# Optimization experiments

Hardware: AMD Instinct MI355X
Metric: run time of the kernel (lower is better)

The kernel has to match this reference:

```python
import jax, jax.numpy as jnp
import numpy as np

N_EMBD = 1024
NUM_HEADS = 16
HEAD_SIZE = 64


def setup_inputs() -> dict:
    key = jax.random.key(0)
    ks = jax.random.split(key, 6)
    B, T, C, hs = 2, 2048, N_EMBD, HEAD_SIZE
    s = 0.02
    return {
        "x": jax.random.normal(ks[0], (B, T, C), dtype=jnp.float32),
        "Wk": jax.random.normal(ks[1], (hs, C), dtype=jnp.float32) * s,  # torch Linear weight [out,in]
        "Wv": jax.random.normal(ks[2], (hs, C), dtype=jnp.float32) * s,
        "Wq": jax.random.normal(ks[3], (C, C), dtype=jnp.float32) * s,
        "Wp": jax.random.normal(ks[4], (C, C), dtype=jnp.float32) * s,
        "bp": jax.random.normal(ks[5], (C,), dtype=jnp.float32) * s,
    }


def reference(x, Wk, Wv, Wq, Wp, bp):
    B, T, C = x.shape
    H, hs = NUM_HEADS, HEAD_SIZE
    k = x @ Wk.T                      # [B,T,hs]
    v = x @ Wv.T                      # [B,T,hs]
    q = x @ Wq.T                      # [B,T,C]
    # Faithful to torch: raw view of [B,T,C] -> [B,H,T,hs] (row-major reshape, not transpose)
    q = q.reshape(B, H, T, hs)
    k = k.reshape(B, 1, T, hs)
    v = v.reshape(B, 1, T, hs)
    att = jnp.einsum("bhqd,bhkd->bhqk", q, jnp.broadcast_to(k, (B, 1, T, hs))) * (hs ** -0.5)
    mask = jnp.tril(jnp.ones((T, T), dtype=bool))[None, None]  # [1,1,T,T]
    att = jnp.where(mask, att, -jnp.inf)
    att = jax.nn.softmax(att, axis=-1)
    y = jnp.einsum("bhqk,bhkd->bhqd", att, jnp.broadcast_to(v, (B, 1, T, hs)))  # [B,H,T,hs]
    y = jnp.transpose(y, (0, 2, 1, 3)).reshape(B, T, C)
    return y @ Wp.T + bp
```

## Files before the change

### kernel.cpp

```cpp
#include <hip/hip_runtime.h>
#include <cstddef>
#include <cstdint>

#define B_N 2
#define T_N 2048
#define C_N 1024
#define H_N 16
#define HS_N 64
#define M_N (B_N * T_N)

typedef __attribute__((ext_vector_type(8))) short bf16x8;
typedef __attribute__((ext_vector_type(4))) float f32x4;

#define QSCALE 0.18033688011112042f

__device__ __forceinline__ ushort f2bf(float f) {
    union { float f; uint32_t u; } v; v.f = f;
    uint32_t r = v.u + 0x7fffu + ((v.u >> 16) & 1u);
    return (ushort)(r >> 16);
}

__global__ void cvt_all_kernel(const float* __restrict__ x,
                               const float* __restrict__ Wq,
                               const float* __restrict__ Wp,
                               const float* __restrict__ Wk,
                               const float* __restrict__ Wv,
                               ushort* __restrict__ xb,
                               ushort* __restrict__ Wqb,
                               ushort* __restrict__ Wpb,
                               ushort* __restrict__ Wkvb) {
    const int S0 = M_N * C_N / 4;
    const int S1 = S0 + C_N * C_N / 4;
    const int S2 = S1 + C_N * C_N / 4;
    const int S3 = S2 + HS_N * C_N / 4;
    const int S4 = S3 + HS_N * C_N / 4;
    const int stride = gridDim.x * blockDim.x;
    for (int i = blockIdx.x * blockDim.x + threadIdx.x; i < S4; i += stride) {
        const float* src; ushort* dst; int j; float sc = 1.f;
        if (i < S0)      { src = x;  dst = xb;   j = i; }
        else if (i < S1) { src = Wq; dst = Wqb;  j = i - S0; sc = QSCALE; }
        else if (i < S2) { src = Wp; dst = Wpb;  j = i - S1; }
        else if (i < S3) { src = Wk; dst = Wkvb; j = i - S2; }
        else             { src = Wv; dst = Wkvb + HS_N * C_N; j = i - S3; }
        const float4 f = ((const float4*)src)[j];
        ushort4 o;
        o.x = f2bf(f.x * sc); o.y = f2bf(f.y * sc);
        o.z = f2bf(f.z * sc); o.w = f2bf(f.w * sc);
        ((ushort4*)dst)[j] = o;
    }
}

template <bool BF16_OUT>
__global__ __launch_bounds__(256) void gemm_bf16_mfma(
    const ushort* __restrict__ A,
    const ushort* __restrict__ W,
    const float* __restrict__ bias,
    void* __restrict__ Cout,
    ushort* __restrict__ Cout2,
    int Nsplit, int N2, int K)
{
    __shared__ ushort As[128][72];
    __shared__ ushort Bs[64][72];
    const int m0 = blockIdx.x * 128;
    const int n0 = blockIdx.y * 64;
    const int tid = threadIdx.x;
    const int wid = tid >> 6;
    const int lane = tid & 63;
    const int ln = lane & 15;
    const int quad = lane >> 4;
    const int wm = wid >> 1, wn = wid & 1;

    f32x4 acc[4][2];
    #pragma unroll
    for (int i = 0; i < 4; ++i)
        #pragma unroll
        for (int j = 0; j < 2; ++j)
            acc[i][j] = (f32x4){0.f, 0.f, 0.f, 0.f};

    const int r0 = tid >> 2;
    const int c0 = tid & 3;
    const ushort* agA = A + (size_t)(m0 + r0) * K + c0 * 8;
    const ushort* agB = A + (size_t)(m0 + r0 + 64) * K + c0 * 8;
    const ushort* wg  = W + (size_t)(n0 + r0) * K + c0 * 8;

    int4 pa0, pa1, pa2, pa3, pb0, pb1;
    {
        pa0 = *(const int4*)(agA);      pa1 = *(const int4*)(agA + 32);
        pa2 = *(const int4*)(agB);      pa3 = *(const int4*)(agB + 32);
        pb0 = *(const int4*)(wg);       pb1 = *(const int4*)(wg + 32);
    }

    for (int k0 = 0; k0 < K; k0 += 64) {
        __syncthreads();
        *(int4*)&As[r0][c0 * 8]           = pa0;
        *(int4*)&As[r0][c0 * 8 + 32]      = pa1;
        *(int4*)&As[r0 + 64][c0 * 8]      = pa2;
        *(int4*)&As[r0 + 64][c0 * 8 + 32] = pa3;
        *(int4*)&Bs[r0][c0 * 8]           = pb0;
        *(int4*)&Bs[r0][c0 * 8 + 32]      = pb1;
        __syncthreads();
        const int kn = k0 + 64;
        if (kn < K) {
            pa0 = *(const int4*)(agA + kn);      pa1 = *(const int4*)(agA + kn + 32);
            pa2 = *(const int4*)(agB + kn);      pa3 = *(const int4*)(agB + kn + 32);
            pb0 = *(const int4*)(wg + kn);       pb1 = *(const int4*)(wg + kn + 32);
        }
        #pragma unroll
        for (int hh = 0; hh < 2; ++hh) {
            bf16x8 af[4], bf[2];
            #pragma unroll
            for (int i = 0; i < 4; ++i)
                af[i] = *(const bf16x8*)&As[wm * 64 + i * 16 + ln][hh * 32 + quad * 8];
            #pragma unroll
            for (int j = 0; j < 2; ++j)
                bf[j] = *(const bf16x8*)&Bs[wn * 32 + j * 16 + ln][hh * 32 + quad * 8];
            #pragma unroll
            for (int i = 0; i < 4; ++i)
                #pragma unroll
                for (int j = 0; j < 2; ++j)
                    acc[i][j] = __builtin_amdgcn_mfma_f32_16x16x32_bf16(
                        af[i], bf[j], acc[i][j], 0, 0, 0);
        }
    }

    const bool side2 = (n0 >= Nsplit);
    #pragma unroll
    for (int i = 0; i < 4; ++i) {
        #pragma unroll
        for (int j = 0; j < 2; ++j) {
            const int col = n0 + wn * 32 + j * 16 + ln;
            const float bv = (!side2 && bias) ? bias[col] : 0.f;
            #pragma unroll
            for (int reg = 0; reg < 4; ++reg) {
                const int row = m0 + wm * 64 + i * 16 + quad * 4 + reg;
                const float v = acc[i][j][reg] + bv;
                if (side2)
                    Cout2[(size_t)row * N2 + (col - Nsplit)] = f2bf(v);
                else if (BF16_OUT)
                    ((ushort*)Cout)[(size_t)row * Nsplit + col] = f2bf(v);
                else
                    ((float*)Cout)[(size_t)row * Nsplit + col] = v;
            }
        }
    }
}

__global__ __launch_bounds__(256) void attn_mfma_kernel(
    const ushort* __restrict__ qb,
    const ushort* __restrict__ kvb,
    ushort* __restrict__ yb)
{
    __shared__ ushort Ks[64][72];
    __shared__ ushort Vt[64][72];
    __shared__ ushort Ps[4][16][72];

    const int bh = blockIdx.x;
    const int b = bh >> 4, h = bh & 15;
    const int p = blockIdx.y;
    const int lastB = 31 - p;
    const int qA0 = p * 64;
    const int qB0 = lastB * 64;
    const int tid = threadIdx.x;
    const int wid = tid >> 6;
    const int lane = tid & 63;
    const int ln = lane & 15;
    const int quad = lane >> 4;

    const ushort* qstrip = qb + (size_t)b * T_N * C_N + (size_t)h * T_N * HS_N;
    const size_t qrA = (size_t)(qA0 + wid * 16 + ln) * HS_N;
    const size_t qrB = (size_t)(qB0 + wid * 16 + ln) * HS_N;
    const bf16x8 qfA0 = *(const bf16x8*)(qstrip + qrA + quad * 8);
    const bf16x8 qfA1 = *(const bf16x8*)(qstrip + qrA + 32 + quad * 8);
    const bf16x8 qfB0 = *(const bf16x8*)(qstrip + qrB + quad * 8);
    const bf16x8 qfB1 = *(const bf16x8*)(qstrip + qrB + 32 + quad * 8);

    f32x4 oA[4], oB[4];
    float lA[4] = {0.f, 0.f, 0.f, 0.f};
    float lB[4] = {0.f, 0.f, 0.f, 0.f};
    #pragma unroll
    for (int nt = 0; nt < 4; ++nt) {
        oA[nt] = (f32x4){0.f, 0.f, 0.f, 0.f};
        oB[nt] = (f32x4){0.f, 0.f, 0.f, 0.f};
    }

    const ushort* kvbase = kvb + (size_t)b * T_N * 128;
    const int rs = tid >> 3;
    const int cs = tid & 7;

    int4 kc0, kc1, vc0, vc1;
    {
        const ushort* g0 = kvbase + (size_t)rs * 128 + cs * 8;
        kc0 = *(const int4*)g0;
        kc1 = *(const int4*)(g0 + 32 * 128);
        vc0 = *(const int4*)(g0 + 64);
        vc1 = *(const int4*)(g0 + 32 * 128 + 64);
    }

    auto compute_tile = [&](const bf16x8& qf0, const bf16x8& qf1,
                            f32x4* o, float* l, int qt0, int k0, bool diag) {
        f32x4 s[4];
        #pragma unroll
        for (int nt = 0; nt < 4; ++nt) {
            s[nt] = (f32x4){0.f, 0.f, 0.f, 0.f};
            const bf16x8 kf0 = *(const bf16x8*)&Ks[nt * 16 + ln][quad * 8];
            const bf16x8 kf1 = *(const bf16x8*)&Ks[nt * 16 + ln][32 + quad * 8];
            s[nt] = __builtin_amdgcn_mfma_f32_16x16x32_bf16(qf0, kf0, s[nt], 0, 0, 0);
            s[nt] = __builtin_amdgcn_mfma_f32_16x16x32_bf16(qf1, kf1, s[nt], 0, 0, 0);
        }
        #pragma unroll
        for (int reg = 0; reg < 4; ++reg) {
            const int qg = qt0 + wid * 16 + quad * 4 + reg;
            const int prow = quad * 4 + reg;
            const int psw = (prow >> 1) & 7;
            #pragma unroll
            for (int nt = 0; nt < 4; ++nt) {
                float sv = s[nt][reg];
                if (diag && (k0 + nt * 16 + ln > qg)) sv = -1e30f;
                const float pe = __builtin_amdgcn_exp2f(sv);
                l[reg] += pe;
                Ps[wid][prow][((2 * nt + (ln >> 3)) ^ psw) * 8 + (ln & 7)] = f2bf(pe);
            }
        }
        #pragma unroll
        for (int ks2 = 0; ks2 < 2; ++ks2) {
            const int rsw = (ln >> 1) & 7;
            const bf16x8 pf = *(const bf16x8*)&Ps[wid][ln][((ks2 * 4 + quad) ^ rsw) * 8];
            #pragma unroll
            for (int nt = 0; nt < 4; ++nt) {
                const int vsw = (2 * nt + (ln >> 3)) & 7;
                const bf16x8 vf = *(const bf16x8*)&Vt[nt * 16 + ln][((quad + 4 * ks2) ^ vsw) * 8];
                o[nt] = __builtin_amdgcn_mfma_f32_16x16x32_bf16(pf, vf, o[nt], 0, 0, 0);
            }
        }
    };

    for (int kt = 0; kt <= lastB; ++kt) {
        const int k0 = kt * 64;
        __syncthreads();
        *(int4*)&Ks[rs][cs * 8] = kc0;
        *(int4*)&Ks[rs + 32][cs * 8] = kc1;
        {
            const ushort* p0 = (const ushort*)&vc0;
            const ushort* p1 = (const ushort*)&vc1;
            const int pc0 = ((rs >> 3) ^ cs) * 8 + (rs & 7);
            const int pc1 = (((rs + 32) >> 3) ^ cs) * 8 + (rs & 7);
            #pragma unroll
            for (int i = 0; i < 8; ++i) {
                Vt[cs * 8 + i][pc0] = p0[i];
                Vt[cs * 8 + i][pc1] = p1[i];
            }
        }
        __syncthreads();
        if (kt < lastB) {
            const ushort* g0 = kvbase + (size_t)(k0 + 64 + rs) * 128 + cs * 8;
            kc0 = *(const int4*)g0;
            kc1 = *(const int4*)(g0 + 32 * 128);
            vc0 = *(const int4*)(g0 + 64);
            vc1 = *(const int4*)(g0 + 32 * 128 + 64);
        }
        compute_tile(qfB0, qfB1, oB, lB, qB0, k0, kt == lastB);
        if (kt <= p)
            compute_tile(qfA0, qfA1, oA, lA, qA0, k0, kt == p);
    }

    #pragma unroll
    for (int reg = 0; reg < 4; ++reg) {
        float la = lA[reg], lb = lB[reg];
        la += __shfl_xor(la, 1); lb += __shfl_xor(lb, 1);
        la += __shfl_xor(la, 2); lb += __shfl_xor(lb, 2);
        la += __shfl_xor(la, 4); lb += __shfl_xor(lb, 4);
        la += __shfl_xor(la, 8); lb += __shfl_xor(lb, 8);
        const float invA = 1.0f / la;
        const float invB = 1.0f / lb;
        const int qgA = qA0 + wid * 16 + quad * 4 + reg;
        const int qgB = qB0 + wid * 16 + quad * 4 + reg;
        ushort* yrA = yb + (size_t)b * T_N * C_N + (size_t)qgA * C_N + h * HS_N;
        ushort* yrB = yb + (size_t)b * T_N * C_N + (size_t)qgB * C_N + h * HS_N;
        #pragma unroll
        for (int nt = 0; nt < 4; ++nt) {
            yrA[nt * 16 + ln] = f2bf(oA[nt][reg] * invA);
            yrB[nt * 16 + ln] = f2bf(oB[nt][reg] * invB);
        }
    }
}

extern "C" void kernel_launch(void* const* d_in, const int* in_sizes, int n_in,
                              void* d_out, int out_size, void* d_ws, size_t ws_size,
                              hipStream_t stream) {
    const float* x  = (const float*)d_in[0];
    const float* Wk = (const float*)d_in[1];
    const float* Wv = (const float*)d_in[2];
    const float* Wq = (const float*)d_in[3];
    const float* Wp = (const float*)d_in[4];
    const float* bp = (const float*)d_in[5];
    float* out = (float*)d_out;

    ushort* xb   = (ushort*)d_ws;
    ushort* qb   = xb   + (size_t)M_N * C_N;
    ushort* yb   = qb   + (size_t)M_N * C_N;
    ushort* kvb  = yb   + (size_t)M_N * C_N;
    ushort* Wqb  = kvb  + (size_t)M_N * 128;
    ushort* Wkvb = Wqb  + (size_t)C_N * C_N;
    ushort* Wpb  = Wkvb + (size_t)128 * C_N;

    cvt_all_kernel<<<1024, 256, 0, stream>>>(x, Wq, Wp, Wk, Wv,
                                             xb, Wqb, Wpb, Wkvb);

    gemm_bf16_mfma<true><<<dim3(M_N / 128, (C_N + 128) / 64), 256, 0, stream>>>(
        xb, Wqb, nullptr, qb, kvb, C_N, 128, C_N);

    attn_mfma_kernel<<<dim3(B_N * H_N, 16), 256, 0, stream>>>(qb, kvb, yb);

    gemm_bf16_mfma<false><<<dim3(M_N / 128, C_N / 64), 256, 0, stream>>>(
        yb, Wpb, bp, out, nullptr, C_N, 0, C_N);
}
```

Baseline: 168.4 us.

## Use direct global-to-LDS loads in GEMM and widen attention query tiles

The GEMM now stages A and W tiles through global_load_lds with an XOR-swizzled unpadded LDS layout, replacing the register prefetch. That removes the register round trip but loses the overlap of next-tile loads with compute. The attention kernel now gives each block two 128-row query strips (two 16-row sub-tiles per wave) and hoists the K/V fragments into registers once per key tile. It also computes S transposed, so P can be written with packed stores. This halves the grid and raises register pressure (launch_bounds 256,1) in exchange for more K/V reuse per LDS load.

```diff
diff --git a/kernel.cpp b/kernel.cpp
--- a/kernel.cpp
+++ b/kernel.cpp
@@ -19,6 +19,11 @@
     uint32_t r = v.u + 0x7fffu + ((v.u >> 16) & 1u);
     return (ushort)(r >> 16);
 }
+
+#define GLL16(g, l)                                                         \
+    __builtin_amdgcn_global_load_lds(                                       \
+        (const __attribute__((address_space(1))) unsigned int*)(g),         \
+        (__attribute__((address_space(3))) unsigned int*)(l), 16, 0, 0)
 
 __global__ void cvt_all_kernel(const float* __restrict__ x,
                                const float* __restrict__ Wq,
@@ -59,8 +64,8 @@
     ushort* __restrict__ Cout2,
     int Nsplit, int N2, int K)
 {
-    __shared__ ushort As[128][72];
-    __shared__ ushort Bs[64][72];
+    __shared__ ushort As[128 * 64];
+    __shared__ ushort Bs[64 * 64];
     const int m0 = blockIdx.x * 128;
     const int n0 = blockIdx.y * 64;
     const int tid = threadIdx.x;
@@ -77,43 +82,39 @@
         for (int j = 0; j < 2; ++j)
             acc[i][j] = (f32x4){0.f, 0.f, 0.f, 0.f};
 
-    const int r0 = tid >> 2;
-    const int c0 = tid & 3;
-    const ushort* agA = A + (size_t)(m0 + r0) * K + c0 * 8;
-    const ushort* agB = A + (size_t)(m0 + r0 + 64) * K + c0 * 8;
-    const ushort* wg  = W + (size_t)(n0 + r0) * K + c0 * 8;
-
-    int4 pa0, pa1, pa2, pa3, pb0, pb1;
-    {
-        pa0 = *(const int4*)(agA);      pa1 = *(const int4*)(agA + 32);
-        pa2 = *(const int4*)(agB);      pa3 = *(const int4*)(agB + 32);
-        pb0 = *(const int4*)(wg);       pb1 = *(const int4*)(wg + 32);
-    }
+    const int srow = lane >> 3;
+    const int schk = (lane & 7) ^ srow;
 
     for (int k0 = 0; k0 < K; k0 += 64) {
         __syncthreads();
-        *(int4*)&As[r0][c0 * 8]           = pa0;
-        *(int4*)&As[r0][c0 * 8 + 32]      = pa1;
-        *(int4*)&As[r0 + 64][c0 * 8]      = pa2;
-        *(int4*)&As[r0 + 64][c0 * 8 + 32] = pa3;
-        *(int4*)&Bs[r0][c0 * 8]           = pb0;
-        *(int4*)&Bs[r0][c0 * 8 + 32]      = pb1;
+        #pragma unroll
+        for (int t = 0; t < 4; ++t) {
+            const int seg = wid * 4 + t;
+            const int row = seg * 8 + srow;
+            GLL16(A + (size_t)(m0 + row) * K + k0 + schk * 8, As + seg * 512);
+        }
+        #pragma unroll
+        for (int t = 0; t < 2; ++t) {
+            const int seg = wid * 2 + t;
+            const int row = seg * 8 + srow;
+            GLL16(W + (size_t)(n0 + row) * K + k0 + schk * 8, Bs + seg * 512);
+        }
         __syncthreads();
-        const int kn = k0 + 64;
-        if (kn < K) {
-            pa0 = *(const int4*)(agA + kn);      pa1 = *(const int4*)(agA + kn + 32);
-            pa2 = *(const int4*)(agB + kn);      pa3 = *(const int4*)(agB + kn + 32);
-            pb0 = *(const int4*)(wg + kn);       pb1 = *(const int4*)(wg + kn + 32);
-        }
+
         #pragma unroll
         for (int hh = 0; hh < 2; ++hh) {
             bf16x8 af[4], bf[2];
-            #pragma unroll
-            for (int i = 0; i < 4; ++i)
-                af[i] = *(const bf16x8*)&As[wm * 64 + i * 16 + ln][hh * 32 + quad * 8];
-            #pragma unroll
-            for (int j = 0; j < 2; ++j)
-                bf[j] = *(const bf16x8*)&Bs[wn * 32 + j * 16 + ln][hh * 32 + quad * 8];
+            const int sw = ln & 7;
+            #pragma unroll
+            for (int i = 0; i < 4; ++i) {
+                const int row = wm * 64 + i * 16 + ln;
+                af[i] = *(const bf16x8*)&As[row * 64 + (((hh * 4 + quad) ^ sw) * 8)];
+            }
+            #pragma unroll
+            for (int j = 0; j < 2; ++j) {
+                const int row = wn * 32 + j * 16 + ln;
+                bf[j] = *(const bf16x8*)&Bs[row * 64 + (((hh * 4 + quad) ^ sw) * 8)];
+            }
             #pragma unroll
             for (int i = 0; i < 4; ++i)
                 #pragma unroll
@@ -145,21 +146,20 @@
     }
 }
 
-__global__ __launch_bounds__(256) void attn_mfma_kernel(
+__global__ __launch_bounds__(256, 1) void attn_mfma_kernel(
     const ushort* __restrict__ qb,
     const ushort* __restrict__ kvb,
     ushort* __restrict__ yb)
 {
     __shared__ ushort Ks[64][72];
     __shared__ ushort Vt[64][72];
-    __shared__ ushort Ps[4][16][72];
+    __shared__ ushort Ps[8][16][72];
 
     const int bh = blockIdx.x;
     const int b = bh >> 4, h = bh & 15;
     const int p = blockIdx.y;
-    const int lastB = 31 - p;
-    const int qA0 = p * 64;
-    const int qB0 = lastB * 64;
+    const int qB0 = (15 - p) * 128;
+    const int qA0 = p * 128;
     const int tid = threadIdx.x;
     const int wid = tid >> 6;
     const int lane = tid & 63;
@@ -167,21 +167,26 @@
     const int quad = lane >> 4;
 
     const ushort* qstrip = qb + (size_t)b * T_N * C_N + (size_t)h * T_N * HS_N;
-    const size_t qrA = (size_t)(qA0 + wid * 16 + ln) * HS_N;
-    const size_t qrB = (size_t)(qB0 + wid * 16 + ln) * HS_N;
-    const bf16x8 qfA0 = *(const bf16x8*)(qstrip + qrA + quad * 8);
-    const bf16x8 qfA1 = *(const bf16x8*)(qstrip + qrA + 32 + quad * 8);
-    const bf16x8 qfB0 = *(const bf16x8*)(qstrip + qrB + quad * 8);
-    const bf16x8 qfB1 = *(const bf16x8*)(qstrip + qrB + 32 + quad * 8);
-
-    f32x4 oA[4], oB[4];
-    float lA[4] = {0.f, 0.f, 0.f, 0.f};
-    float lB[4] = {0.f, 0.f, 0.f, 0.f};
-    #pragma unroll
-    for (int nt = 0; nt < 4; ++nt) {
-        oA[nt] = (f32x4){0.f, 0.f, 0.f, 0.f};
-        oB[nt] = (f32x4){0.f, 0.f, 0.f, 0.f};
-    }
+    const int qbase[2] = {qB0, qA0};
+    bf16x8 qf[2][2][2];
+    #pragma unroll
+    for (int t = 0; t < 2; ++t)
+        #pragma unroll
+        for (int s = 0; s < 2; ++s) {
+            const size_t r = (size_t)(qbase[t] + wid * 32 + s * 16 + ln) * HS_N;
+            qf[t][s][0] = *(const bf16x8*)(qstrip + r + quad * 8);
+            qf[t][s][1] = *(const bf16x8*)(qstrip + r + 32 + quad * 8);
+        }
+
+    f32x4 o[2][2][4];
+    float l_i[2][2] = {{0.f, 0.f}, {0.f, 0.f}};
+    #pragma unroll
+    for (int t = 0; t < 2; ++t)
+        #pragma unroll
+        for (int s = 0; s < 2; ++s)
+            #pragma unroll
+            for (int nt = 0; nt < 4; ++nt)
+                o[t][s][nt] = (f32x4){0.f, 0.f, 0.f, 0.f};
 
     const ushort* kvbase = kvb + (size_t)b * T_N * 128;
     const int rs = tid >> 3;
@@ -196,45 +201,51 @@
         vc1 = *(const int4*)(g0 + 32 * 128 + 64);
     }
 
-    auto compute_tile = [&](const bf16x8& qf0, const bf16x8& qf1,
-                            f32x4* o, float* l, int qt0, int k0, bool diag) {
-        f32x4 s[4];
-        #pragma unroll
-        for (int nt = 0; nt < 4; ++nt) {
-            s[nt] = (f32x4){0.f, 0.f, 0.f, 0.f};
-            const bf16x8 kf0 = *(const bf16x8*)&Ks[nt * 16 + ln][quad * 8];
-            const bf16x8 kf1 = *(const bf16x8*)&Ks[nt * 16 + ln][32 + quad * 8];
-            s[nt] = __builtin_amdgcn_mfma_f32_16x16x32_bf16(qf0, kf0, s[nt], 0, 0, 0);
-            s[nt] = __builtin_amdgcn_mfma_f32_16x16x32_bf16(qf1, kf1, s[nt], 0, 0, 0);
-        }
-        #pragma unroll
-        for (int reg = 0; reg < 4; ++reg) {
-            const int qg = qt0 + wid * 16 + quad * 4 + reg;
-            const int prow = quad * 4 + reg;
-            const int psw = (prow >> 1) & 7;
+    bf16x8 kf[4][2], vf[4][2];
+
+    auto tile_compute = [&](int t, int qt0, int k0) {
+        #pragma unroll
+        for (int s = 0; s < 2; ++s) {
+            const int qg = qt0 + wid * 32 + s * 16 + ln;
+            f32x4 sc[4];
             #pragma unroll
             for (int nt = 0; nt < 4; ++nt) {
-                float sv = s[nt][reg];
-                if (diag && (k0 + nt * 16 + ln > qg)) sv = -1e30f;
-                const float pe = __builtin_amdgcn_exp2f(sv);
-                l[reg] += pe;
-                Ps[wid][prow][((2 * nt + (ln >> 3)) ^ psw) * 8 + (ln & 7)] = f2bf(pe);
-            }
-        }
-        #pragma unroll
-        for (int ks2 = 0; ks2 < 2; ++ks2) {
-            const int rsw = (ln >> 1) & 7;
-            const bf16x8 pf = *(const bf16x8*)&Ps[wid][ln][((ks2 * 4 + quad) ^ rsw) * 8];
+                sc[nt] = (f32x4){0.f, 0.f, 0.f, 0.f};
+                sc[nt] = __builtin_amdgcn_mfma_f32_16x16x32_bf16(
+                    kf[nt][0], qf[t][s][0], sc[nt], 0, 0, 0);
+                sc[nt] = __builtin_amdgcn_mfma_f32_16x16x32_bf16(
+                    kf[nt][1], qf[t][s][1], sc[nt], 0, 0, 0);
+            }
+            const bool dg = (k0 + 63 > qt0 + wid * 32 + s * 16);
+            const int plane = wid * 2 + s;
             #pragma unroll
             for (int nt = 0; nt < 4; ++nt) {
-                const int vsw = (2 * nt + (ln >> 3)) & 7;
-                const bf16x8 vf = *(const bf16x8*)&Vt[nt * 16 + ln][((quad + 4 * ks2) ^ vsw) * 8];
-                o[nt] = __builtin_amdgcn_mfma_f32_16x16x32_bf16(pf, vf, o[nt], 0, 0, 0);
+                ushort pk[4];
+                #pragma unroll
+                for (int reg = 0; reg < 4; ++reg) {
+                    const int key = k0 + nt * 16 + quad * 4 + reg;
+                    float sv = sc[nt][reg];
+                    if (dg && key > qg) sv = -1e30f;
+                    const float pe = __builtin_amdgcn_exp2f(sv);
+                    l_i[t][s] += pe;
+                    pk[reg] = f2bf(pe);
+                }
+                *(uint2*)&Ps[plane][ln][nt * 16 + quad * 4] = *(uint2*)pk;
+            }
+            #pragma unroll
+            for (int ks2 = 0; ks2 < 2; ++ks2) {
+                const bf16x8 pf =
+                    *(const bf16x8*)&Ps[plane][ln][ks2 * 32 + quad * 8];
+                #pragma unroll
+                for (int nt = 0; nt < 4; ++nt)
+                    o[t][s][nt] = __builtin_amdgcn_mfma_f32_16x16x32_bf16(
+                        pf, vf[nt][ks2], o[t][s][nt], 0, 0, 0);
             }
         }
     };
 
-    for (int kt = 0; kt <= lastB; ++kt) {
+    const int nkt = 2 * (16 - p);
+    for (int kt = 0; kt < nkt; ++kt) {
         const int k0 = kt * 64;
         __syncthreads();
         *(int4*)&Ks[rs][cs * 8] = kc0;
@@ -251,35 +262,46 @@
             }
         }
         __syncthreads();
-        if (kt < lastB) {
+        if (kt + 1 < nkt) {
             const ushort* g0 = kvbase + (size_t)(k0 + 64 + rs) * 128 + cs * 8;
             kc0 = *(const int4*)g0;
             kc1 = *(const int4*)(g0 + 32 * 128);
             vc0 = *(const int4*)(g0 + 64);
             vc1 = *(const int4*)(g0 + 32 * 128 + 64);
         }
-        compute_tile(qfB0, qfB1, oB, lB, qB0, k0, kt == lastB);
-        if (kt <= p)
-            compute_tile(qfA0, qfA1, oA, lA, qA0, k0, kt == p);
-    }
-
-    #pragma unroll
-    for (int reg = 0; reg < 4; ++reg) {
-        float la = lA[reg], lb = lB[reg];
-        la += __shfl_xor(la, 1); lb += __shfl_xor(lb, 1);
-        la += __shfl_xor(la, 2); lb += __shfl_xor(lb, 2);
-        la += __shfl_xor(la, 4); lb += __shfl_xor(lb, 4);
-        la += __shfl_xor(la, 8); lb += __shfl_xor(lb, 8);
-        const float invA = 1.0f / la;
-        const float invB = 1.0f / lb;
-        const int qgA = qA0 + wid * 16 + quad * 4 + reg;
-        const int qgB = qB0 + wid * 16 + quad * 4 + reg;
-        ushort* yrA = yb + (size_t)b * T_N * C_N + (size_t)qgA * C_N + h * HS_N;
-        ushort* yrB = yb + (size_t)b * T_N * C_N + (size_t)qgB * C_N + h * HS_N;
         #pragma unroll
         for (int nt = 0; nt < 4; ++nt) {
-            yrA[nt * 16 + ln] = f2bf(oA[nt][reg] * invA);
-            yrB[nt * 16 + ln] = f2bf(oB[nt][reg] * invB);
+            kf[nt][0] = *(const bf16x8*)&Ks[nt * 16 + ln][quad * 8];
+            kf[nt][1] = *(const bf16x8*)&Ks[nt * 16 + ln][32 + quad * 8];
+            #pragma unroll
+            for (int ks2 = 0; ks2 < 2; ++ks2) {
+                const int vsw = (2 * nt + (ln >> 3)) & 7;
+                vf[nt][ks2] =
+                    *(const bf16x8*)&Vt[nt * 16 + ln][((quad + 4 * ks2) ^ vsw) * 8];
+            }
+        }
+        tile_compute(0, qB0, k0);
+        if (kt <= 2 * p + 1)
+            tile_compute(1, qA0, k0);
+    }
+
+    #pragma unroll
+    for (int t = 0; t < 2; ++t) {
+        #pragma unroll
+        for (int s = 0; s < 2; ++s) {
+            float l = l_i[t][s];
+            l += __shfl_xor(l, 16);
+            l += __shfl_xor(l, 32);
+            #pragma unroll
+            for (int reg = 0; reg < 4; ++reg) {
+                const float inv = 1.0f / __shfl(l, quad * 4 + reg);
+                const int qg = qbase[t] + wid * 32 + s * 16 + quad * 4 + reg;
+                ushort* yrow = yb + (size_t)b * T_N * C_N + (size_t)qg * C_N
+                               + h * HS_N;
+                #pragma unroll
+                for (int nt = 0; nt < 4; ++nt)
+                    yrow[nt * 16 + ln] = f2bf(o[t][s][nt][reg] * inv);
+            }
         }
     }
 }
@@ -309,7 +331,7 @@
     gemm_bf16_mfma<true><<<dim3(M_N / 128, (C_N + 128) / 64), 256, 0, stream>>>(
         xb, Wqb, nullptr, qb, kvb, C_N, 128, C_N);
 
-    attn_mfma_kernel<<<dim3(B_N * H_N, 16), 256, 0, stream>>>(qb, kvb, yb);
+    attn_mfma_kernel<<<dim3(B_N * H_N, 8), 256, 0, stream>>>(qb, kvb, yb);
 
     gemm_bf16_mfma<false><<<dim3(M_N / 128, C_N / 64), 256, 0, stream>>>(
         yb, Wpb, bp, out, nullptr, C_N, 0, C_N);
```

New measurement: 169.2 us. No clear change (+0.5%).
